# Kernel tuning notes

Hardware: AMD Instinct MI355X
Metric: run time of the kernel (lower is better)

## Reference

```python
import jax, jax.numpy as jnp
import numpy as np

B, NB, BIN = 8, 512, 10           # batch, num_bins, bin_size
D, H, L, F, E, K = 1024, 8, 4, 1024, 30, 4  # emb, heads, layers, ffn, experts, top_k
S = NB + 1                        # seq len with CLS token
DH = D // H
CAP = 1152


def _pos_encoding(seq, d):
    pos = np.arange(seq)[:, None].astype(np.float32)
    div = np.exp(np.arange(0, d, 2).astype(np.float32) * (-np.log(10000.0) / d))
    pe = np.zeros((seq, d), dtype=np.float32)
    pe[:, 0::2] = np.sin(pos * div)
    pe[:, 1::2] = np.cos(pos * div)
    return jnp.asarray(pe)

PE = _pos_encoding(S, D)


def _ln(h, g, b):
    m = h.mean(-1, keepdims=True)
    v = ((h - m) ** 2).mean(-1, keepdims=True)
    return (h - m) * jax.lax.rsqrt(v + 1e-5) * g + b


def _conv(h, w, dil):
    # torch Conv1d(k=3, padding=dil, dilation=dil, bias=False) -> same length
    return jax.lax.conv_general_dilated(h, w, (1,), [(dil, dil)], rhs_dilation=(dil,),
                                        dimension_numbers=('NCH', 'OIH', 'NCH'))


def _moe(m, Wg, Bg, W1, B1, W2, B2):
    # top-k routed expert FFN with capacity-based dispatch (no dense all-expert compute)
    T = B * S
    xt = m.reshape(T, D)
    probs = jax.nn.softmax(xt @ Wg + Bg, axis=-1)           # [T, E]
    gate, idx = jax.lax.top_k(probs, K)                     # [T, K]
    gate = gate / gate.sum(-1, keepdims=True)
    e = idx.reshape(-1)                                     # [T*K]
    g = gate.reshape(-1)
    oh = jax.nn.one_hot(e, E, dtype=jnp.int32)
    pos = (jnp.cumsum(oh, axis=0) * oh).sum(-1) - 1         # position within expert
    keep = pos < CAP
    pos_c = jnp.where(keep, pos, CAP)                       # overflow -> dummy slot CAP
    xt_rep = xt[jnp.repeat(jnp.arange(T), K)]               # [T*K, D]
    buf = jnp.zeros((E, CAP + 1, D), m.dtype).at[e, pos_c].add(xt_rep)
    hid = jax.nn.gelu(jnp.einsum('ecd,edf->ecf', buf, W1) + B1[:, None, :], approximate=False)
    out = jnp.einsum('ecf,efd->ecd', hid, W2) + B2[:, None, :]
    y = out[e, pos_c] * (g * keep)[:, None]                 # dropped tokens masked to 0
    return y.reshape(T, K, D).sum(1).reshape(B, S, D)


def _layer(h, p):
    (l1g, l1b, l2g, l2b, Wq, Wk, Wv, Wo, Bq, Bk, Bv, Bo, Wg, Bg, We1, Be1, We2, Be2) = p
    a = _ln(h, l1g, l1b)
    q = (a @ Wq + Bq).reshape(B, S, H, DH)
    k = (a @ Wk + Bk).reshape(B, S, H, DH)
    v = (a @ Wv + Bv).reshape(B, S, H, DH)
    att = jax.nn.softmax(jnp.einsum('bqhd,bkhd->bhqk', q, k) / np.sqrt(DH), axis=-1)
    o = jnp.einsum('bhqk,bkhd->bqhd', att, v).reshape(B, S, D) @ Wo + Bo
    h = h + o
    m = _ln(h, l2g, l2b)
    h = h + _moe(m, Wg, Bg, We1, Be1, We2, Be2)
    return h, None


def _fwd(x, conv_w1, conv_w2, conv_w3, bn1_g, bn1_b, bn2_g, bn2_b, bn3_g, bn3_b,
         proj_w, proj_b, cls_token, mask_token, ln1_g, ln1_b, ln2_g, ln2_b,
         wq, wk, wv, wo, bq, bk, bv, bo, wg, bg, we1, be1, we2, be2):
    x3 = x.reshape(B, NB, BIN)
    h = x3.reshape(B * NB, 1, BIN)
    bn_scale = np.float32(1.0 / np.sqrt(1.0 + 1e-5))  # eval BN: running mean 0, var 1
    for w, gm, bt, dil in ((conv_w1, bn1_g, bn1_b, 1), (conv_w2, bn2_g, bn2_b, 2), (conv_w3, bn3_g, bn3_b, 4)):
        h = _conv(h, w, dil)
        h = h * (gm * bn_scale)[None, :, None] + bt[None, :, None]
        h = jax.nn.gelu(h, approximate=False)
    h = h.mean(-1)                                   # AdaptiveAvgPool1d(1)
    emb = (h @ proj_w + proj_b).reshape(B, NB, D)
    msk = jnp.all(x3 == -100.0, axis=-1)[..., None]
    emb = jnp.where(msk, mask_token, emb)
    emb = jnp.concatenate([jnp.broadcast_to(cls_token, (B, 1, D)), emb], axis=1)
    emb = emb + PE[None]
    h, _ = jax.lax.scan(_layer, emb, (ln1_g, ln1_b, ln2_g, ln2_b, wq, wk, wv, wo,
                                      bq, bk, bv, bo, wg, bg, we1, be1, we2, be2))
    return h[:, 0, :]


def setup_inputs() -> dict:
    key = jax.random.key(0)
    ks = iter(jax.random.split(key, 40))
    r = lambda shape, s=0.02: jax.random.normal(next(ks), shape, jnp.float32) * s
    return dict(
        x=jax.random.normal(next(ks), (B, NB * BIN), jnp.float32),
        conv_w1=r((16, 1, 3), 0.3), conv_w2=r((32, 16, 3), 0.15), conv_w3=r((64, 32, 3), 0.1),
        bn1_g=jnp.ones((16,)), bn1_b=jnp.zeros((16,)),
        bn2_g=jnp.ones((32,)), bn2_b=jnp.zeros((32,)),
        bn3_g=jnp.ones((64,)), bn3_b=jnp.zeros((64,)),
        proj_w=r((64, D), 0.05), proj_b=jnp.zeros((D,)),
        cls_token=r((1, 1, D)), mask_token=r((1, 1, D)),
        ln1_g=jnp.ones((L, D)), ln1_b=jnp.zeros((L, D)),
        ln2_g=jnp.ones((L, D)), ln2_b=jnp.zeros((L, D)),
        wq=r((L, D, D)), wk=r((L, D, D)), wv=r((L, D, D)), wo=r((L, D, D)),
        bq=jnp.zeros((L, D)), bk=jnp.zeros((L, D)), bv=jnp.zeros((L, D)), bo=jnp.zeros((L, D)),
        wg=r((L, D, E)), bg=jnp.zeros((L, E)),
        we1=r((L, E, D, F)), be1=jnp.zeros((L, E, F)),
        we2=r((L, E, F, D)), be2=jnp.zeros((L, E, D)),
    )


def reference(x, conv_w1, conv_w2, conv_w3, bn1_g, bn1_b, bn2_g, bn2_b, bn3_g, bn3_b,
              proj_w, proj_b, cls_token, mask_token, ln1_g, ln1_b, ln2_g, ln2_b,
              wq, wk, wv, wo, bq, bk, bv, bo, wg, bg, we1, be1, we2, be2):
    return _fwd(x, conv_w1, conv_w2, conv_w3, bn1_g, bn1_b, bn2_g, bn2_b, bn3_g, bn3_b,
                proj_w, proj_b, cls_token, mask_token, ln1_g, ln1_b, ln2_g, ln2_b,
                wq, wk, wv, wo, bq, bk, bv, bo, wg, bg, we1, be1, we2, be2)
```

## Files before the change

### kernel.cpp

```cpp
#include <hip/hip_runtime.h>
#include <hip/hip_bf16.h>
#include <math.h>

#define BATCH   8
#define NBINS   512
#define BINSZ   10
#define DMODEL  1024
#define NHEAD   8
#define DHEAD   128
#define NLAYER  4
#define NEXP    30
#define TOPK    4
#define SEQ     513
#define NTOK    (BATCH*SEQ)
#define NBINTOT (BATCH*NBINS)
#define CAPACITY 1152
#define TKF     (NTOK*TOPK)

typedef __attribute__((ext_vector_type(8))) __bf16 bf16x8;
typedef __attribute__((ext_vector_type(4))) float f32x4;

__device__ __forceinline__ float gelu_f(float x) {
  return 0.5f * x * (1.0f + erff(x * 0.7071067811865475f));
}

#define CSTEP(acc, T, DIL, hr, wA, wB, wC) { \
  float vv_ = (wB) * (hr)[T]; \
  if ((T) >= (DIL)) vv_ = fmaf((wA), (hr)[(T)-(DIL)], vv_); \
  if ((T) + (DIL) <= 9) vv_ = fmaf((wC), (hr)[(T)+(DIL)], vv_); \
  acc += vv_; }

#define CALL10(DIL, hr, wA, wB, wC) \
  CSTEP(t0,0,DIL,hr,wA,wB,wC); CSTEP(t1,1,DIL,hr,wA,wB,wC); \
  CSTEP(t2,2,DIL,hr,wA,wB,wC); CSTEP(t3,3,DIL,hr,wA,wB,wC); \
  CSTEP(t4,4,DIL,hr,wA,wB,wC); CSTEP(t5,5,DIL,hr,wA,wB,wC); \
  CSTEP(t6,6,DIL,hr,wA,wB,wC); CSTEP(t7,7,DIL,hr,wA,wB,wC); \
  CSTEP(t8,8,DIL,hr,wA,wB,wC); CSTEP(t9,9,DIL,hr,wA,wB,wC);

#define ZERO10 float t0=0.f,t1=0.f,t2=0.f,t3=0.f,t4=0.f,t5=0.f,t6=0.f,t7=0.f,t8=0.f,t9=0.f;

#define STORE10(dst, sc, sh) \
  (dst)[0]=gelu_f(t0*(sc)+(sh)); (dst)[1]=gelu_f(t1*(sc)+(sh)); \
  (dst)[2]=gelu_f(t2*(sc)+(sh)); (dst)[3]=gelu_f(t3*(sc)+(sh)); \
  (dst)[4]=gelu_f(t4*(sc)+(sh)); (dst)[5]=gelu_f(t5*(sc)+(sh)); \
  (dst)[6]=gelu_f(t6*(sc)+(sh)); (dst)[7]=gelu_f(t7*(sc)+(sh)); \
  (dst)[8]=gelu_f(t8*(sc)+(sh)); (dst)[9]=gelu_f(t9*(sc)+(sh));

__global__ __launch_bounds__(64) void conv_frontend(const float* __restrict__ x,
                              const float* __restrict__ w1, const float* __restrict__ w2,
                              const float* __restrict__ w3,
                              const float* __restrict__ g1, const float* __restrict__ b1,
                              const float* __restrict__ g2, const float* __restrict__ b2,
                              const float* __restrict__ g3, const float* __restrict__ b3,
                              float* __restrict__ feat, int* __restrict__ msk) {
  const float bnscale = 0.9999950000374997f;
  int bin = blockIdx.x;
  int c = threadIdx.x;
  __shared__ float xs[BINSZ];
  __shared__ float h1[16][BINSZ];
  __shared__ float h2[32][BINSZ];
  if (c < BINSZ) xs[c] = x[bin*BINSZ + c];
  if (c == 0) {
    int all = 1;
    for (int t = 0; t < BINSZ; t++) if (x[bin*BINSZ+t] != -100.0f) { all = 0; break; }
    msk[bin] = all;
  }
  __syncthreads();
  if (c < 16) {
    float sc = g1[c]*bnscale, sh = b1[c];
    float wA = w1[c*3], wB = w1[c*3+1], wC = w1[c*3+2];
    const float* hr = &xs[0];
    ZERO10;
    CALL10(1, hr, wA, wB, wC);
    STORE10(&h1[c][0], sc, sh);
  }
  __syncthreads();
  if (c < 32) {
    float sc = g2[c]*bnscale, sh = b2[c];
    ZERO10;
    for (int ci = 0; ci < 16; ci++) {
      const float* w = w2 + (c*16+ci)*3;
      float wA = w[0], wB = w[1], wC = w[2];
      const float* hr = &h1[ci][0];
      CALL10(2, hr, wA, wB, wC);
    }
    STORE10(&h2[c][0], sc, sh);
  }
  __syncthreads();
  {
    float sc = g3[c]*bnscale, sh = b3[c];
    ZERO10;
    for (int ci = 0; ci < 32; ci++) {
      const float* w = w3 + (c*32+ci)*3;
      float wA = w[0], wB = w[1], wC = w[2];
      const float* hr = &h2[ci][0];
      CALL10(4, hr, wA, wB, wC);
    }
    float mean = gelu_f(t0*sc+sh) + gelu_f(t1*sc+sh) + gelu_f(t2*sc+sh)
               + gelu_f(t3*sc+sh) + gelu_f(t4*sc+sh) + gelu_f(t5*sc+sh)
               + gelu_f(t6*sc+sh) + gelu_f(t7*sc+sh) + gelu_f(t8*sc+sh)
               + gelu_f(t9*sc+sh);
    feat[bin*64 + c] = mean * 0.1f;
  }
}

__global__ void embed_kernel(const float* __restrict__ feat, const int* __restrict__ msk,
                             const float* __restrict__ proj_w, const float* __restrict__ proj_b,
                             const float* __restrict__ cls_token, const float* __restrict__ mask_token,
                             float* __restrict__ h) {
  int s_ = blockIdx.x;
  int b  = blockIdx.y;
  int tid = threadIdx.x;
  __shared__ __align__(16) float fs[64];
  float out[4];
  if (s_ == 0) {
#pragma unroll
    for (int u = 0; u < 4; u++) out[u] = cls_token[tid*4+u];
  } else {
    int bin = b*NBINS + (s_-1);
    if (tid < 16) ((float4*)fs)[tid] = ((const float4*)(feat + (size_t)bin*64))[tid];
    __syncthreads();
    int m_ = msk[bin];
#pragma unroll
    for (int u = 0; u < 4; u++) {
      int d = tid*4+u;
      float acc = proj_b[d];
      for (int ci = 0; ci < 64; ci++) acc = fmaf(fs[ci], proj_w[ci*DMODEL + d], acc);
      out[u] = m_ ? mask_token[d] : acc;
    }
  }
  const float c0 = -0.008994473019507992f;
#pragma unroll
  for (int u = 0; u < 4; u++) {
    int d = tid*4+u;
    float div = expf(c0 * (float)(d & ~1));
    float ang = (float)s_ * div;
    float pe = (d & 1) ? cosf(ang) : sinf(ang);
    h[((size_t)(b*SEQ + s_))*DMODEL + d] = out[u] + pe;
  }
}

__global__ void ln_kernel(const float* __restrict__ x, float* __restrict__ out,
                          const float* __restrict__ g, const float* __restrict__ b) {
  int t = blockIdx.x, tid = threadIdx.x;
  float4 v = ((const float4*)(x + (size_t)t*DMODEL))[tid];
  float s  = v.x+v.y+v.z+v.w;
  float sq = v.x*v.x+v.y*v.y+v.z*v.z+v.w*v.w;
  for (int off = 32; off; off >>= 1) { s += __shfl_down(s, off); sq += __shfl_down(sq, off); }
  __shared__ float ss[4], ssq[4], mv[2];
  int w = tid >> 6, l = tid & 63;
  if (l == 0) { ss[w] = s; ssq[w] = sq; }
  __syncthreads();
  if (tid == 0) {
    float a = 0, c = 0;
    for (int i = 0; i < 4; i++) { a += ss[i]; c += ssq[i]; }
    float mean = a * (1.f/DMODEL);
    float var  = c * (1.f/DMODEL) - mean*mean;
    mv[0] = mean; mv[1] = rsqrtf(var + 1e-5f);
  }
  __syncthreads();
  float mean = mv[0], inv = mv[1];
  float4 gg = ((const float4*)g)[tid];
  float4 bb = ((const float4*)b)[tid];
  float4 o;
  o.x = (v.x-mean)*inv*gg.x + bb.x;
  o.y = (v.y-mean)*inv*gg.y + bb.y;
  o.z = (v.z-mean)*inv*gg.z + bb.z;
  o.w = (v.w-mean)*inv*gg.w + bb.w;
  ((float4*)(out + (size_t)t*DMODEL))[tid] = o;
}

template<int MODE>
__global__ __launch_bounds__(512) void gemm_bf16(
    const float* __restrict__ A, const float* __restrict__ W,
    const float* __restrict__ bias, float* __restrict__ C, int M,
    const int* __restrict__ rowmap, const int* __restrict__ cnt,
    const float* __restrict__ gate) {
  int tid = threadIdx.x;
  int rowbase, validrows, e = 0;
  const float* Wb = W;
  if (MODE <= 1) {
    rowbase = blockIdx.x * 128;
    validrows = M - rowbase; if (validrows > 128) validrows = 128;
  } else {
    e = blockIdx.x / 9;
    int p0 = (blockIdx.x % 9) * 128;
    int ce = cnt[e];
    if (p0 >= ce) return;
    rowbase = p0;
    validrows = ce - p0; if (validrows > 128) validrows = 128;
    Wb = W + (size_t)e * 1024 * 1024;
  }
  int colbase = blockIdx.y * 128;

  __shared__ __align__(16) __bf16 As[4][128][8];
  __shared__ __align__(16) __bf16 Bs[4][128][8];
  __shared__ int srcrow[128];
  __shared__ int frow[128];

  if (tid < 128) {
    if (MODE <= 1) { srcrow[tid] = rowbase + tid; frow[tid] = rowbase + tid; }
    else if (tid < validrows) {
      int f = rowmap[e*CAPACITY + rowbase + tid];
      frow[tid] = f;
      srcrow[tid] = (MODE == 2) ? (f >> 2) : f;
    } else { frow[tid] = 0; srcrow[tid] = 0; }
  }
  __syncthreads();

  int arow = tid >> 2, ag = tid & 3;
  int wcol = tid & 127, wgp = tid >> 7;
  bool aval = (arow < validrows);
  const float* Ap = A + (size_t)srcrow[arow] * 1024 + ag * 8;
  const float* Wp = Wb + (size_t)(wgp * 8) * 1024 + colbase + wcol;

  int w  = tid >> 6;
  int wr = w & 3, wc = w >> 2;
  int l  = tid & 63;
  int lr = l & 15, lg = l >> 4;

  f32x4 acc[2][4] = {};

  float4 a_lo = {}, a_hi = {};
  float wreg[8];
  if (aval) { a_lo = *(const float4*)(Ap); a_hi = *(const float4*)(Ap + 4); }
#pragma unroll
  for (int j = 0; j < 8; j++) wreg[j] = Wp[(size_t)j * 1024];

  for (int kt = 0; kt < 1024; kt += 32) {
    __syncthreads();
    bf16x8 av;
    av[0] = (__bf16)a_lo.x; av[1] = (__bf16)a_lo.y; av[2] = (__bf16)a_lo.z; av[3] = (__bf16)a_lo.w;
    av[4] = (__bf16)a_hi.x; av[5] = (__bf16)a_hi.y; av[6] = (__bf16)a_hi.z; av[7] = (__bf16)a_hi.w;
    *(bf16x8*)&As[ag][arow][0] = av;
    bf16x8 bv;
#pragma unroll
    for (int j = 0; j < 8; j++) bv[j] = (__bf16)wreg[j];
    *(bf16x8*)&Bs[wgp][wcol][0] = bv;
    __syncthreads();

    if (kt + 32 < 1024) {
      if (aval) {
        a_lo = *(const float4*)(Ap + kt + 32);
        a_hi = *(const float4*)(Ap + kt + 36);
      }
#pragma unroll
      for (int j = 0; j < 8; j++) wreg[j] = Wp[(size_t)(kt + 32 + j) * 1024];
    }

    bf16x8 af[2], bf[4];
    af[0] = *(const bf16x8*)&As[lg][wr*32 + lr][0];
    af[1] = *(const bf16x8*)&As[lg][wr*32 + 16 + lr][0];
#pragma unroll
    for (int fj = 0; fj < 4; fj++) bf[fj] = *(const bf16x8*)&Bs[lg][wc*64 + fj*16 + lr][0];
#pragma unroll
    for (int fi = 0; fi < 2; fi++)
#pragma unroll
      for (int fj = 0; fj < 4; fj++)
        acc[fi][fj] = __builtin_amdgcn_mfma_f32_16x16x32_bf16(af[fi], bf[fj], acc[fi][fj], 0, 0, 0);
  }

  const float* bptr = (MODE >= 2) ? (bias + (size_t)e * 1024) : bias;
#pragma unroll
  for (int fj = 0; fj < 4; fj++) {
    int col = wc*64 + fj*16 + lr;
    float bvv = bptr[colbase + col];
#pragma unroll
    for (int fi = 0; fi < 2; fi++) {
#pragma unroll
      for (int i = 0; i < 4; i++) {
        int r = wr*32 + fi*16 + lg*4 + i;
        if (r >= validrows) continue;
        float val = acc[fi][fj][i] + bvv;
        if (MODE == 0) {
          C[(size_t)(rowbase + r)*1024 + colbase + col] = val;
        } else if (MODE == 1) {
          float* p = C + (size_t)(rowbase + r)*1024 + colbase + col;
          *p = *p + val;
        } else if (MODE == 2) {
          C[(size_t)frow[r]*1024 + colbase + col] = gelu_f(val);
        } else {
          C[(size_t)frow[r]*1024 + colbase + col] = gate[frow[r]] * val;
        }
      }
    }
  }
}

__global__ __launch_bounds__(256) void attn_mfma(const float* __restrict__ q,
                                                 const float* __restrict__ k,
                                                 const float* __restrict__ v,
                                                 float* __restrict__ o) {
  int qt = blockIdx.x;
  int bh = blockIdx.y;
  int b = bh >> 3, hh = bh & 7;
  int tid = threadIdx.x;
  int wid = tid >> 6, l = tid & 63;
  int lr = l & 15, lg = l >> 4;

  __shared__ __align__(16) __bf16 Ks[64*128];
  __shared__ __align__(16) __bf16 Vt[128*64];

  const float scale = 0.08838834764831845f;

  int qtok = qt*64 + wid*16 + lr;
  int qtokc = qtok < SEQ ? qtok : SEQ-1;
  const float* qrow = q + ((size_t)(b*SEQ + qtokc))*DMODEL + hh*DHEAD;
  bf16x8 qf[4];
#pragma unroll
  for (int c = 0; c < 4; c++) {
    float4 x0 = *(const float4*)(qrow + c*32 + lg*8);
    float4 x1 = *(const float4*)(qrow + c*32 + lg*8 + 4);
    bf16x8 t;
    t[0]=(__bf16)x0.x; t[1]=(__bf16)x0.y; t[2]=(__bf16)x0.z; t[3]=(__bf16)x0.w;
    t[4]=(__bf16)x1.x; t[5]=(__bf16)x1.y; t[6]=(__bf16)x1.z; t[7]=(__bf16)x1.w;
    qf[c] = t;
  }

  float mreg = -1e30f, lsum = 0.f;
  f32x4 Oacc[8] = {};

  int krow = tid & 63, kdc = tid >> 6;
  int vd = tid & 127, vkg0 = tid >> 7;

  for (int kt = 0; kt < 9; kt++) {
    int kt0 = kt*64;
    __syncthreads();
    {
      int tok = kt0 + krow; if (tok >= SEQ) tok = SEQ-1;
      const float* kr = k + ((size_t)(b*SEQ + tok))*DMODEL + hh*DHEAD + kdc*32;
#pragma unroll
      for (int s2 = 0; s2 < 4; s2++) {
        float4 a0 = *(const float4*)(kr + s2*8);
        float4 a1 = *(const float4*)(kr + s2*8 + 4);
        bf16x8 t;
        t[0]=(__bf16)a0.x; t[1]=(__bf16)a0.y; t[2]=(__bf16)a0.z; t[3]=(__bf16)a0.w;
        t[4]=(__bf16)a1.x; t[5]=(__bf16)a1.y; t[6]=(__bf16)a1.z; t[7]=(__bf16)a1.w;
        int byte = (krow*256 + (kdc*32 + s2*8)*2) ^ ((krow & 7) << 4);
        *(bf16x8*)((char*)Ks + byte) = t;
      }
    }
    {
#pragma unroll
      for (int it = 0; it < 4; it++) {
        int kkg = vkg0 + it*2;
        bf16x8 t;
#pragma unroll
        for (int j = 0; j < 8; j++) {
          int tok = kt0 + kkg*8 + j; if (tok >= SEQ) tok = SEQ-1;
          t[j] = (__bf16)v[((size_t)(b*SEQ + tok))*DMODEL + hh*DHEAD + vd];
        }
        int byte = (vd*128 + kkg*16) ^ ((vd & 7) << 4);
        *(bf16x8*)((char*)Vt + byte) = t;
      }
    }
    __syncthreads();

    f32x4 sacc[4] = {};
#pragma unroll
    for (int c = 0; c < 4; c++) {
#pragma unroll
      for (int jb = 0; jb < 4; jb++) {
        int row = jb*16 + lr;
        int byte = (row*256 + (c*32 + lg*8)*2) ^ ((lr & 7) << 4);
        bf16x8 af = *(const bf16x8*)((const char*)Ks + byte);
        sacc[jb] = __builtin_amdgcn_mfma_f32_16x16x32_bf16(af, qf[c], sacc[jb], 0, 0, 0);
      }
    }

    float sv[4][4];
    float mt = -1e30f;
#pragma unroll
    for (int jb = 0; jb < 4; jb++)
#pragma unroll
      for (int i = 0; i < 4; i++) {
        int kkI = kt0 + jb*16 + lg*4 + i;
        float s = sacc[jb][i] * scale;
        if (kkI >= SEQ) s = -1e30f;
        sv[jb][i] = s;
        mt = fmaxf(mt, s);
      }
    mt = fmaxf(mt, __shfl_xor(mt, 16));
    mt = fmaxf(mt, __shfl_xor(mt, 32));
    float mnew = fmaxf(mreg, mt);
    float alpha = expf(mreg - mnew);
    float rs = 0.f;
#pragma unroll
    for (int jb = 0; jb < 4; jb++)
#pragma unroll
      for (int i = 0; i < 4; i++) {
        float p = expf(sv[jb][i] - mnew);
        sv[jb][i] = p; rs += p;
      }
    rs += __shfl_xor(rs, 16);
    rs += __shfl_xor(rs, 32);
    lsum = lsum * alpha + rs;
    mreg = mnew;

    unsigned pk[4][2];
#pragma unroll
    for (int jb = 0; jb < 4; jb++) {
      unsigned short c0 = __builtin_bit_cast(unsigned short, (__bf16)sv[jb][0]);
      unsigned short c1 = __builtin_bit_cast(unsigned short, (__bf16)sv[jb][1]);
      unsigned short c2 = __builtin_bit_cast(unsigned short, (__bf16)sv[jb][2]);
      unsigned short c3 = __builtin_bit_cast(unsigned short, (__bf16)sv[jb][3]);
      pk[jb][0] = ((unsigned)c1 << 16) | c0;
      pk[jb][1] = ((unsigned)c3 << 16) | c2;
    }

    float al0 = __shfl(alpha, lg*4 + 0);
    float al1 = __shfl(alpha, lg*4 + 1);
    float al2 = __shfl(alpha, lg*4 + 2);
    float al3 = __shfl(alpha, lg*4 + 3);
#pragma unroll
    for (int db = 0; db < 8; db++) {
      Oacc[db][0] *= al0; Oacc[db][1] *= al1; Oacc[db][2] *= al2; Oacc[db][3] *= al3;
    }

    int srcA = lr + ((lg & 1) << 5);
    int srcB = srcA + 16;
    bool hiSel = (lg >> 1) != 0;
#pragma unroll
    for (int c = 0; c < 2; c++) {
      int a00 = __shfl((int)pk[2*c][0], srcA);
      int a01 = __shfl((int)pk[2*c][1], srcA);
      int a10 = __shfl((int)pk[2*c+1][0], srcA);
      int a11 = __shfl((int)pk[2*c+1][1], srcA);
      int b00 = __shfl((int)pk[2*c][0], srcB);
      int b01 = __shfl((int)pk[2*c][1], srcB);
      int b10 = __shfl((int)pk[2*c+1][0], srcB);
      int b11 = __shfl((int)pk[2*c+1][1], srcB);
      int4 pa;
      pa.x = hiSel ? a10 : a00;
      pa.y = hiSel ? a11 : a01;
      pa.z = hiSel ? b10 : b00;
      pa.w = hiSel ? b11 : b01;
      bf16x8 paf = __builtin_bit_cast(bf16x8, pa);
#pragma unroll
      for (int db = 0; db < 8; db++) {
        int d = db*16 + lr;
        int byte = (d*128 + (c*32 + lg*8)*2) ^ ((lr & 7) << 4);
        bf16x8 bfv = *(const bf16x8*)((const char*)Vt + byte);
        Oacc[db] = __builtin_amdgcn_mfma_f32_16x16x32_bf16(paf, bfv, Oacc[db], 0, 0, 0);
      }
    }
  }

  float l0 = __shfl(lsum, lg*4 + 0);
  float l1 = __shfl(lsum, lg*4 + 1);
  float l2 = __shfl(lsum, lg*4 + 2);
  float l3 = __shfl(lsum, lg*4 + 3);
  float inv[4] = {1.f/l0, 1.f/l1, 1.f/l2, 1.f/l3};
#pragma unroll
  for (int i = 0; i < 4; i++) {
    int tok = qt*64 + wid*16 + lg*4 + i;
    if (tok < SEQ) {
      float* dst = o + ((size_t)(b*SEQ + tok))*DMODEL + hh*DHEAD + lr;
#pragma unroll
      for (int db = 0; db < 8; db++) dst[db*16] = Oacc[db][i] * inv[i];
    }
  }
}

__global__ void moe_gate(const float* __restrict__ m, const float* __restrict__ wg,
                         const float* __restrict__ bg, int* __restrict__ idx,
                         float* __restrict__ gate) {
  int t = blockIdx.x, tid = threadIdx.x;
  __shared__ __align__(16) float xs[DMODEL];
  __shared__ float probs[32];
  ((float4*)xs)[tid] = ((const float4*)(m + (size_t)t*DMODEL))[tid];
  __syncthreads();
  int e = tid >> 3, sub = tid & 7;
  if (e < NEXP) {
    float p = 0.f;
    for (int d = sub; d < DMODEL; d += 8) p = fmaf(xs[d], wg[d*NEXP + e], p);
    p += __shfl_down(p, 4, 8);
    p += __shfl_down(p, 2, 8);
    p += __shfl_down(p, 1, 8);
    if (sub == 0) probs[e] = p + bg[e];
  }
  __syncthreads();
  if (tid == 0) {
    float mx = probs[0];
    for (int i = 1; i < NEXP; i++) mx = fmaxf(mx, probs[i]);
    float ssum = 0.f;
    for (int i = 0; i < NEXP; i++) { probs[i] = expf(probs[i]-mx); ssum += probs[i]; }
    float invs = 1.f / ssum;
    float gv[TOPK]; int gi[TOPK]; float gsum = 0.f;
    for (int kk = 0; kk < TOPK; kk++) {
      float best = -1.f; int bi = 0;
      for (int i = 0; i < NEXP; i++) if (probs[i] > best) { best = probs[i]; bi = i; }
      gv[kk] = best * invs; gi[kk] = bi; probs[bi] = -1.f; gsum += gv[kk];
    }
    float ginv = 1.f / gsum;
    for (int kk = 0; kk < TOPK; kk++) { idx[t*TOPK+kk] = gi[kk]; gate[t*TOPK+kk] = gv[kk]*ginv; }
  }
}

__global__ void moe_dispatch(const int* __restrict__ idx, int* __restrict__ slot,
                             int* __restrict__ rowmap, int* __restrict__ cnt) {
  int e = blockIdx.x, tid = threadIdx.x;
  int lane = tid & 63, wid = tid >> 6;
  __shared__ int wsum[4];
  int base = 0;
  for (int c0 = 0; c0 < TKF; c0 += 256) {
    int f = c0 + tid;
    int match = (f < TKF && idx[f] == e) ? 1 : 0;
    unsigned long long bal = __ballot(match);
    if (lane == 0) wsum[wid] = __popcll(bal);
    __syncthreads();
    int prefix = 0;
#pragma unroll
    for (int w2 = 0; w2 < 4; w2++) if (w2 < wid) prefix += wsum[w2];
    int total = wsum[0] + wsum[1] + wsum[2] + wsum[3];
    if (match) {
      int pos = base + prefix + __popcll(bal & ((1ull << lane) - 1ull));
      if (pos < CAPACITY) { slot[f] = pos; rowmap[e*CAPACITY + pos] = f; }
      else slot[f] = -1;
    }
    base += total;
    __syncthreads();
  }
  if (tid == 0) cnt[e] = (base < CAPACITY) ? base : CAPACITY;
}

__global__ void moe_sum(const float* __restrict__ y, const int* __restrict__ slot,
                        float* __restrict__ h) {
  int t = blockIdx.x, d4 = threadIdx.x;
  float4 acc = ((float4*)(h + (size_t)t*DMODEL))[d4];
#pragma unroll
  for (int kk = 0; kk < TOPK; kk++) {
    int f = t*TOPK + kk;
    if (slot[f] >= 0) {
      float4 yv = ((const float4*)(y + (size_t)f*DMODEL))[d4];
      acc.x += yv.x; acc.y += yv.y; acc.z += yv.z; acc.w += yv.w;
    }
  }
  ((float4*)(h + (size_t)t*DMODEL))[d4] = acc;
}

__global__ void final_copy(const float* __restrict__ h, float* __restrict__ out) {
  int b = blockIdx.x, tid = threadIdx.x;
  float4 v = ((const float4*)(h + (size_t)b*SEQ*DMODEL))[tid];
  ((float4*)(out + (size_t)b*DMODEL))[tid] = v;
}

extern "C" void kernel_launch(void* const* d_in, const int* in_sizes, int n_in,
                              void* d_out, int out_size, void* d_ws, size_t ws_size,
                              hipStream_t stream) {
  (void)in_sizes; (void)n_in; (void)out_size; (void)ws_size;
  const float* x         = (const float*)d_in[0];
  const float* conv_w1   = (const float*)d_in[1];
  const float* conv_w2   = (const float*)d_in[2];
  const float* conv_w3   = (const float*)d_in[3];
  const float* bn1_g     = (const float*)d_in[4];
  const float* bn1_b     = (const float*)d_in[5];
  const float* bn2_g     = (const float*)d_in[6];
  const float* bn2_b     = (const float*)d_in[7];
  const float* bn3_g     = (const float*)d_in[8];
  const float* bn3_b     = (const float*)d_in[9];
  const float* proj_w    = (const float*)d_in[10];
  const float* proj_b    = (const float*)d_in[11];
  const float* cls_token = (const float*)d_in[12];
  const float* mask_tok  = (const float*)d_in[13];
  const float* ln1_g     = (const float*)d_in[14];
  const float* ln1_b     = (const float*)d_in[15];
  const float* ln2_g     = (const float*)d_in[16];
  const float* ln2_b     = (const float*)d_in[17];
  const float* wq        = (const float*)d_in[18];
  const float* wk        = (const float*)d_in[19];
  const float* wv        = (const float*)d_in[20];
  const float* wo        = (const float*)d_in[21];
  const float* bq        = (const float*)d_in[22];
  const float* bk        = (const float*)d_in[23];
  const float* bv        = (const float*)d_in[24];
  const float* bo        = (const float*)d_in[25];
  const float* wg        = (const float*)d_in[26];
  const float* bg        = (const float*)d_in[27];
  const float* we1       = (const float*)d_in[28];
  const float* be1       = (const float*)d_in[29];
  const float* we2       = (const float*)d_in[30];
  const float* be2       = (const float*)d_in[31];
  float* out = (float*)d_out;

  float* ws = (float*)d_ws;
  const size_t TD = (size_t)NTOK * DMODEL;
  float* h    = ws;
  float* xbuf = ws + TD;
  float* qb   = ws + 2*TD;
  float* kb   = ws + 3*TD;
  float* vb   = ws + 4*TD;
  float* ao   = ws + 5*TD;
  float* hid  = ws + 2*TD;
  float* yb   = ws + 6*TD;
  float* feat = ws + 10*TD;
  float* gate = feat + (size_t)NBINTOT*64;
  int* idx    = (int*)(gate + TKF);
  int* slot   = idx + TKF;
  int* rowmap = slot + TKF;
  int* cnt    = rowmap + NEXP*CAPACITY;
  int* msk    = cnt + 32;

  conv_frontend<<<NBINTOT, 64, 0, stream>>>(x, conv_w1, conv_w2, conv_w3,
      bn1_g, bn1_b, bn2_g, bn2_b, bn3_g, bn3_b, feat, msk);
  embed_kernel<<<dim3(SEQ, BATCH), 256, 0, stream>>>(feat, msk, proj_w, proj_b,
      cls_token, mask_tok, h);

  dim3 gdense((NTOK + 127)/128, 8);
  dim3 gmoe(NEXP*9, 8);

  for (int l = 0; l < NLAYER; l++) {
    const float* wq_l = wq + (size_t)l*DMODEL*DMODEL;
    const float* wk_l = wk + (size_t)l*DMODEL*DMODEL;
    const float* wv_l = wv + (size_t)l*DMODEL*DMODEL;
    const float* wo_l = wo + (size_t)l*DMODEL*DMODEL;
    const float* we1_l = we1 + (size_t)l*NEXP*DMODEL*1024;
    const float* we2_l = we2 + (size_t)l*NEXP*1024*DMODEL;

    ln_kernel<<<NTOK, 256, 0, stream>>>(h, xbuf, ln1_g + (size_t)l*DMODEL, ln1_b + (size_t)l*DMODEL);
    gemm_bf16<0><<<gdense, 512, 0, stream>>>(xbuf, wq_l, bq + (size_t)l*DMODEL, qb, NTOK, nullptr, nullptr, nullptr);
    gemm_bf16<0><<<gdense, 512, 0, stream>>>(xbuf, wk_l, bk + (size_t)l*DMODEL, kb, NTOK, nullptr, nullptr, nullptr);
    gemm_bf16<0><<<gdense, 512, 0, stream>>>(xbuf, wv_l, bv + (size_t)l*DMODEL, vb, NTOK, nullptr, nullptr, nullptr);
    attn_mfma<<<dim3(9, BATCH*NHEAD), 256, 0, stream>>>(qb, kb, vb, ao);
    gemm_bf16<1><<<gdense, 512, 0, stream>>>(ao, wo_l, bo + (size_t)l*DMODEL, h, NTOK, nullptr, nullptr, nullptr);
    ln_kernel<<<NTOK, 256, 0, stream>>>(h, xbuf, ln2_g + (size_t)l*DMODEL, ln2_b + (size_t)l*DMODEL);
    moe_gate<<<NTOK, 256, 0, stream>>>(xbuf, wg + (size_t)l*DMODEL*NEXP, bg + (size_t)l*NEXP, idx, gate);
    moe_dispatch<<<NEXP, 256, 0, stream>>>(idx, slot, rowmap, cnt);
    gemm_bf16<2><<<gmoe, 512, 0, stream>>>(xbuf, we1_l, be1 + (size_t)l*NEXP*1024, hid, 0, rowmap, cnt, nullptr);
    gemm_bf16<3><<<gmoe, 512, 0, stream>>>(hid, we2_l, be2 + (size_t)l*NEXP*1024, yb, 0, rowmap, cnt, gate);
    moe_sum<<<NTOK, 256, 0, stream>>>(yb, slot, h);
  }
  final_copy<<<BATCH, 256, 0, stream>>>(h, out);
}
```

Baseline: 3.000 ms.

## Store activations and transposed weights in bf16 to halve GEMM and attention traffic

Adds a per-call kernel that transposes every weight matrix to K-contiguous bf16 layout. The layernorm also writes a bf16 copy of its output. GEMMs, attention and the MoE hidden buffer now read and write bf16 intermediates, so the per-tile float-to-bf16 conversions disappear and strided weight loads become vector loads. The cost is a transpose pass over all weights on every call (about 1 GB of fp32 read), extra workspace, and bf16 rounding of q/k/v and hidden activations.

```diff
diff --git a/kernel.cpp b/kernel.cpp
--- a/kernel.cpp
+++ b/kernel.cpp
@@ -18,10 +18,42 @@
 #define TKF     (NTOK*TOPK)
 
 typedef __attribute__((ext_vector_type(8))) __bf16 bf16x8;
+typedef __attribute__((ext_vector_type(4))) __bf16 bf16x4;
 typedef __attribute__((ext_vector_type(4))) float f32x4;
 
 __device__ __forceinline__ float gelu_f(float x) {
   return 0.5f * x * (1.0f + erff(x * 0.7071067811865475f));
+}
+
+__device__ __forceinline__ bf16x8 bf8_zero() {
+  int4 z = make_int4(0, 0, 0, 0);
+  return __builtin_bit_cast(bf16x8, z);
+}
+
+__global__ __launch_bounds__(256) void transpose_w(const float* __restrict__ src,
+                                                   __bf16* __restrict__ dst) {
+  int mat = blockIdx.y;
+  int tile = blockIdx.x;
+  int kt = (tile >> 4) * 64;
+  int nt = (tile & 15) * 64;
+  const float* s = src + (size_t)mat * 1024 * 1024;
+  __bf16* d = dst + (size_t)mat * 1024 * 1024;
+  __shared__ float t[64][65];
+  int tid = threadIdx.x;
+  int r = tid >> 4, c4 = (tid & 15) * 4;
+#pragma unroll
+  for (int i = 0; i < 4; i++) {
+    float4 v = *(const float4*)(s + (size_t)(kt + r + i*16) * 1024 + nt + c4);
+    t[r + i*16][c4+0] = v.x; t[r + i*16][c4+1] = v.y;
+    t[r + i*16][c4+2] = v.z; t[r + i*16][c4+3] = v.w;
+  }
+  __syncthreads();
+  int r2 = tid >> 2, c2 = (tid & 3) * 16;
+  bf16x8 o0, o1;
+#pragma unroll
+  for (int j = 0; j < 8; j++) { o0[j] = (__bf16)t[c2+j][r2]; o1[j] = (__bf16)t[c2+8+j][r2]; }
+  *(bf16x8*)(d + (size_t)(nt + r2) * 1024 + kt + c2)     = o0;
+  *(bf16x8*)(d + (size_t)(nt + r2) * 1024 + kt + c2 + 8) = o1;
 }
 
 #define CSTEP(acc, T, DIL, hr, wA, wB, wC) { \
@@ -141,6 +173,7 @@
 }
 
 __global__ void ln_kernel(const float* __restrict__ x, float* __restrict__ out,
+                          __bf16* __restrict__ outb,
                           const float* __restrict__ g, const float* __restrict__ b) {
   int t = blockIdx.x, tid = threadIdx.x;
   float4 v = ((const float4*)(x + (size_t)t*DMODEL))[tid];
@@ -168,17 +201,20 @@
   o.z = (v.z-mean)*inv*gg.z + bb.z;
   o.w = (v.w-mean)*inv*gg.w + bb.w;
   ((float4*)(out + (size_t)t*DMODEL))[tid] = o;
+  bf16x4 ob;
+  ob[0] = (__bf16)o.x; ob[1] = (__bf16)o.y; ob[2] = (__bf16)o.z; ob[3] = (__bf16)o.w;
+  *(bf16x4*)(outb + (size_t)t*DMODEL + tid*4) = ob;
 }
 
 template<int MODE>
 __global__ __launch_bounds__(512) void gemm_bf16(
-    const float* __restrict__ A, const float* __restrict__ W,
-    const float* __restrict__ bias, float* __restrict__ C, int M,
+    const __bf16* __restrict__ A, const __bf16* __restrict__ Wt,
+    const float* __restrict__ bias, void* __restrict__ C, int M,
     const int* __restrict__ rowmap, const int* __restrict__ cnt,
     const float* __restrict__ gate) {
   int tid = threadIdx.x;
   int rowbase, validrows, e = 0;
-  const float* Wb = W;
+  const __bf16* Wb = Wt;
   if (MODE <= 1) {
     rowbase = blockIdx.x * 128;
     validrows = M - rowbase; if (validrows > 128) validrows = 128;
@@ -189,7 +225,7 @@
     if (p0 >= ce) return;
     rowbase = p0;
     validrows = ce - p0; if (validrows > 128) validrows = 128;
-    Wb = W + (size_t)e * 1024 * 1024;
+    Wb = Wt + (size_t)e * 1024 * 1024;
   }
   int colbase = blockIdx.y * 128;
 
@@ -211,8 +247,8 @@
   int arow = tid >> 2, ag = tid & 3;
   int wcol = tid & 127, wgp = tid >> 7;
   bool aval = (arow < validrows);
-  const float* Ap = A + (size_t)srcrow[arow] * 1024 + ag * 8;
-  const float* Wp = Wb + (size_t)(wgp * 8) * 1024 + colbase + wcol;
+  const __bf16* Ap = A + (size_t)srcrow[arow] * 1024 + ag * 8;
+  const __bf16* Wp = Wb + (size_t)(colbase + wcol) * 1024 + wgp * 8;
 
   int w  = tid >> 6;
   int wr = w & 3, wc = w >> 2;
@@ -221,31 +257,19 @@
 
   f32x4 acc[2][4] = {};
 
-  float4 a_lo = {}, a_hi = {};
-  float wreg[8];
-  if (aval) { a_lo = *(const float4*)(Ap); a_hi = *(const float4*)(Ap + 4); }
-#pragma unroll
-  for (int j = 0; j < 8; j++) wreg[j] = Wp[(size_t)j * 1024];
+  bf16x8 areg = bf8_zero(), breg;
+  if (aval) areg = *(const bf16x8*)(Ap);
+  breg = *(const bf16x8*)(Wp);
 
   for (int kt = 0; kt < 1024; kt += 32) {
     __syncthreads();
-    bf16x8 av;
-    av[0] = (__bf16)a_lo.x; av[1] = (__bf16)a_lo.y; av[2] = (__bf16)a_lo.z; av[3] = (__bf16)a_lo.w;
-    av[4] = (__bf16)a_hi.x; av[5] = (__bf16)a_hi.y; av[6] = (__bf16)a_hi.z; av[7] = (__bf16)a_hi.w;
-    *(bf16x8*)&As[ag][arow][0] = av;
-    bf16x8 bv;
-#pragma unroll
-    for (int j = 0; j < 8; j++) bv[j] = (__bf16)wreg[j];
-    *(bf16x8*)&Bs[wgp][wcol][0] = bv;
+    *(bf16x8*)&As[ag][arow][0] = areg;
+    *(bf16x8*)&Bs[wgp][wcol][0] = breg;
     __syncthreads();
 
     if (kt + 32 < 1024) {
-      if (aval) {
-        a_lo = *(const float4*)(Ap + kt + 32);
-        a_hi = *(const float4*)(Ap + kt + 36);
-      }
-#pragma unroll
-      for (int j = 0; j < 8; j++) wreg[j] = Wp[(size_t)(kt + 32 + j) * 1024];
+      if (aval) areg = *(const bf16x8*)(Ap + kt + 32);
+      breg = *(const bf16x8*)(Wp + kt + 32);
     }
 
     bf16x8 af[2], bf[4];
@@ -273,24 +297,24 @@
         if (r >= validrows) continue;
         float val = acc[fi][fj][i] + bvv;
         if (MODE == 0) {
-          C[(size_t)(rowbase + r)*1024 + colbase + col] = val;
+          ((__bf16*)C)[(size_t)(rowbase + r)*1024 + colbase + col] = (__bf16)val;
         } else if (MODE == 1) {
-          float* p = C + (size_t)(rowbase + r)*1024 + colbase + col;
+          float* p = (float*)C + (size_t)(rowbase + r)*1024 + colbase + col;
           *p = *p + val;
         } else if (MODE == 2) {
-          C[(size_t)frow[r]*1024 + colbase + col] = gelu_f(val);
+          ((__bf16*)C)[(size_t)frow[r]*1024 + colbase + col] = (__bf16)gelu_f(val);
         } else {
-          C[(size_t)frow[r]*1024 + colbase + col] = gate[frow[r]] * val;
+          ((float*)C)[(size_t)frow[r]*1024 + colbase + col] = gate[frow[r]] * val;
         }
       }
     }
   }
 }
 
-__global__ __launch_bounds__(256) void attn_mfma(const float* __restrict__ q,
-                                                 const float* __restrict__ k,
-                                                 const float* __restrict__ v,
-                                                 float* __restrict__ o) {
+__global__ __launch_bounds__(256) void attn_mfma(const __bf16* __restrict__ q,
+                                                 const __bf16* __restrict__ k,
+                                                 const __bf16* __restrict__ v,
+                                                 __bf16* __restrict__ o) {
   int qt = blockIdx.x;
   int bh = blockIdx.y;
   int b = bh >> 3, hh = bh & 7;
@@ -305,17 +329,10 @@
 
   int qtok = qt*64 + wid*16 + lr;
   int qtokc = qtok < SEQ ? qtok : SEQ-1;
-  const float* qrow = q + ((size_t)(b*SEQ + qtokc))*DMODEL + hh*DHEAD;
+  const __bf16* qrow = q + ((size_t)(b*SEQ + qtokc))*DMODEL + hh*DHEAD;
   bf16x8 qf[4];
 #pragma unroll
-  for (int c = 0; c < 4; c++) {
-    float4 x0 = *(const float4*)(qrow + c*32 + lg*8);
-    float4 x1 = *(const float4*)(qrow + c*32 + lg*8 + 4);
-    bf16x8 t;
-    t[0]=(__bf16)x0.x; t[1]=(__bf16)x0.y; t[2]=(__bf16)x0.z; t[3]=(__bf16)x0.w;
-    t[4]=(__bf16)x1.x; t[5]=(__bf16)x1.y; t[6]=(__bf16)x1.z; t[7]=(__bf16)x1.w;
-    qf[c] = t;
-  }
+  for (int c = 0; c < 4; c++) qf[c] = *(const bf16x8*)(qrow + c*32 + lg*8);
 
   float mreg = -1e30f, lsum = 0.f;
   f32x4 Oacc[8] = {};
@@ -328,14 +345,10 @@
     __syncthreads();
     {
       int tok = kt0 + krow; if (tok >= SEQ) tok = SEQ-1;
-      const float* kr = k + ((size_t)(b*SEQ + tok))*DMODEL + hh*DHEAD + kdc*32;
+      const __bf16* kr = k + ((size_t)(b*SEQ + tok))*DMODEL + hh*DHEAD + kdc*32;
 #pragma unroll
       for (int s2 = 0; s2 < 4; s2++) {
-        float4 a0 = *(const float4*)(kr + s2*8);
-        float4 a1 = *(const float4*)(kr + s2*8 + 4);
-        bf16x8 t;
-        t[0]=(__bf16)a0.x; t[1]=(__bf16)a0.y; t[2]=(__bf16)a0.z; t[3]=(__bf16)a0.w;
-        t[4]=(__bf16)a1.x; t[5]=(__bf16)a1.y; t[6]=(__bf16)a1.z; t[7]=(__bf16)a1.w;
+        bf16x8 t = *(const bf16x8*)(kr + s2*8);
         int byte = (krow*256 + (kdc*32 + s2*8)*2) ^ ((krow & 7) << 4);
         *(bf16x8*)((char*)Ks + byte) = t;
       }
@@ -348,7 +361,7 @@
 #pragma unroll
         for (int j = 0; j < 8; j++) {
           int tok = kt0 + kkg*8 + j; if (tok >= SEQ) tok = SEQ-1;
-          t[j] = (__bf16)v[((size_t)(b*SEQ + tok))*DMODEL + hh*DHEAD + vd];
+          t[j] = v[((size_t)(b*SEQ + tok))*DMODEL + hh*DHEAD + vd];
         }
         int byte = (vd*128 + kkg*16) ^ ((vd & 7) << 4);
         *(bf16x8*)((char*)Vt + byte) = t;
@@ -455,9 +468,9 @@
   for (int i = 0; i < 4; i++) {
     int tok = qt*64 + wid*16 + lg*4 + i;
     if (tok < SEQ) {
-      float* dst = o + ((size_t)(b*SEQ + tok))*DMODEL + hh*DHEAD + lr;
-#pragma unroll
-      for (int db = 0; db < 8; db++) dst[db*16] = Oacc[db][i] * inv[i];
+      __bf16* dst = o + ((size_t)(b*SEQ + tok))*DMODEL + hh*DHEAD + lr;
+#pragma unroll
+      for (int db = 0; db < 8; db++) dst[db*16] = (__bf16)(Oacc[db][i] * inv[i]);
     }
   }
 }
@@ -583,23 +596,40 @@
   const float* be2       = (const float*)d_in[31];
   float* out = (float*)d_out;
 
-  float* ws = (float*)d_ws;
-  const size_t TD = (size_t)NTOK * DMODEL;
-  float* h    = ws;
-  float* xbuf = ws + TD;
-  float* qb   = ws + 2*TD;
-  float* kb   = ws + 3*TD;
-  float* vb   = ws + 4*TD;
-  float* ao   = ws + 5*TD;
-  float* hid  = ws + 2*TD;
-  float* yb   = ws + 6*TD;
-  float* feat = ws + 10*TD;
-  float* gate = feat + (size_t)NBINTOT*64;
-  int* idx    = (int*)(gate + TKF);
-  int* slot   = idx + TKF;
-  int* rowmap = slot + TKF;
-  int* cnt    = rowmap + NEXP*CAPACITY;
-  int* msk    = cnt + 32;
+  char* base = (char*)d_ws;
+  const size_t TDB = (size_t)NTOK * DMODEL * 4;
+  float*  h    = (float*)(base);
+  float*  xbuf = (float*)(base + TDB);
+  float*  yb   = (float*)(base + 2*TDB);
+  __bf16* xbf  = (__bf16*)(base + 6*TDB);
+  __bf16* qb   = (__bf16*)(base + 6*TDB + TDB/2);
+  __bf16* kb   = (__bf16*)(base + 7*TDB);
+  __bf16* vb   = (__bf16*)(base + 7*TDB + TDB/2);
+  __bf16* ao   = (__bf16*)(base + 8*TDB);
+  __bf16* hid  = (__bf16*)(base + 8*TDB + TDB/2);
+  char* misc   = base + 11*TDB;
+  float* feat  = (float*)misc;
+  float* gate  = feat + (size_t)NBINTOT*64;
+  int* idx     = (int*)(gate + TKF);
+  int* slot    = idx + TKF;
+  int* rowmap  = slot + TKF;
+  int* cnt     = rowmap + NEXP*CAPACITY;
+  int* msk     = cnt + 32;
+  char* wtb    = base + 12*TDB;
+  const size_t MB1 = (size_t)1024*1024;
+  __bf16* wtq  = (__bf16*)wtb;
+  __bf16* wtk  = wtq + 4*MB1;
+  __bf16* wtv  = wtk + 4*MB1;
+  __bf16* wto  = wtv + 4*MB1;
+  __bf16* wte1 = wto + 4*MB1;
+  __bf16* wte2 = wte1 + 120*MB1;
+
+  transpose_w<<<dim3(256, 4),   256, 0, stream>>>(wq,  wtq);
+  transpose_w<<<dim3(256, 4),   256, 0, stream>>>(wk,  wtk);
+  transpose_w<<<dim3(256, 4),   256, 0, stream>>>(wv,  wtv);
+  transpose_w<<<dim3(256, 4),   256, 0, stream>>>(wo,  wto);
+  transpose_w<<<dim3(256, 120), 256, 0, stream>>>(we1, wte1);
+  transpose_w<<<dim3(256, 120), 256, 0, stream>>>(we2, wte2);
 
   conv_frontend<<<NBINTOT, 64, 0, stream>>>(x, conv_w1, conv_w2, conv_w3,
       bn1_g, bn1_b, bn2_g, bn2_b, bn3_g, bn3_b, feat, msk);
@@ -610,24 +640,25 @@
   dim3 gmoe(NEXP*9, 8);
 
   for (int l = 0; l < NLAYER; l++) {
-    const float* wq_l = wq + (size_t)l*DMODEL*DMODEL;
-    const float* wk_l = wk + (size_t)l*DMODEL*DMODEL;
-    const float* wv_l = wv + (size_t)l*DMODEL*DMODEL;
-    const float* wo_l = wo + (size_t)l*DMODEL*DMODEL;
-    const float* we1_l = we1 + (size_t)l*NEXP*DMODEL*1024;
-    const float* we2_l = we2 + (size_t)l*NEXP*1024*DMODEL;
-
-    ln_kernel<<<NTOK, 256, 0, stream>>>(h, xbuf, ln1_g + (size_t)l*DMODEL, ln1_b + (size_t)l*DMODEL);
-    gemm_bf16<0><<<gdense, 512, 0, stream>>>(xbuf, wq_l, bq + (size_t)l*DMODEL, qb, NTOK, nullptr, nullptr, nullptr);
-    gemm_bf16<0><<<gdense, 512, 0, stream>>>(xbuf, wk_l, bk + (size_t)l*DMODEL, kb, NTOK, nullptr, nullptr, nullptr);
-    gemm_bf16<0><<<gdense, 512, 0, stream>>>(xbuf, wv_l, bv + (size_t)l*DMODEL, vb, NTOK, nullptr, nullptr, nullptr);
+    for (int z = 0; z < 1; z++) {}
+    __bf16* wtq_l = wtq + (size_t)l*MB1;
+    __bf16* wtk_l = wtk + (size_t)l*MB1;
+    __bf16* wtv_l = wtv + (size_t)l*MB1;
+    __bf16* wto_l = wto + (size_t)l*MB1;
+    __bf16* wte1_l = wte1 + (size_t)l*NEXP*MB1;
+    __bf16* wte2_l = wte2 + (size_t)l*NEXP*MB1;
+
+    ln_kernel<<<NTOK, 256, 0, stream>>>(h, xbuf, xbf, ln1_g + (size_t)l*DMODEL, ln1_b + (size_t)l*DMODEL);
+    gemm_bf16<0><<<gdense, 512, 0, stream>>>(xbf, wtq_l, bq + (size_t)l*DMODEL, qb, NTOK, nullptr, nullptr, nullptr);
+    gemm_bf16<0><<<gdense, 512, 0, stream>>>(xbf, wtk_l, bk + (size_t)l*DMODEL, kb, NTOK, nullptr, nullptr, nullptr);
+    gemm_bf16<0><<<gdense, 512, 0, stream>>>(xbf, wtv_l, bv + (size_t)l*DMODEL, vb, NTOK, nullptr, nullptr, nullptr);
     attn_mfma<<<dim3(9, BATCH*NHEAD), 256, 0, stream>>>(qb, kb, vb, ao);
-    gemm_bf16<1><<<gdense, 512, 0, stream>>>(ao, wo_l, bo + (size_t)l*DMODEL, h, NTOK, nullptr, nullptr, nullptr);
-    ln_kernel<<<NTOK, 256, 0, stream>>>(h, xbuf, ln2_g + (size_t)l*DMODEL, ln2_b + (size_t)l*DMODEL);
+    gemm_bf16<1><<<gdense, 512, 0, stream>>>(ao, wto_l, bo + (size_t)l*DMODEL, h, NTOK, nullptr, nullptr, nullptr);
+    ln_kernel<<<NTOK, 256, 0, stream>>>(h, xbuf, xbf, ln2_g + (size_t)l*DMODEL, ln2_b + (size_t)l*DMODEL);
     moe_gate<<<NTOK, 256, 0, stream>>>(xbuf, wg + (size_t)l*DMODEL*NEXP, bg + (size_t)l*NEXP, idx, gate);
     moe_dispatch<<<NEXP, 256, 0, stream>>>(idx, slot, rowmap, cnt);
-    gemm_bf16<2><<<gmoe, 512, 0, stream>>>(xbuf, we1_l, be1 + (size_t)l*NEXP*1024, hid, 0, rowmap, cnt, nullptr);
-    gemm_bf16<3><<<gmoe, 512, 0, stream>>>(hid, we2_l, be2 + (size_t)l*NEXP*1024, yb, 0, rowmap, cnt, gate);
+    gemm_bf16<2><<<gmoe, 512, 0, stream>>>(xbf, wte1_l, be1 + (size_t)l*NEXP*1024, hid, 0, rowmap, cnt, nullptr);
+    gemm_bf16<3><<<gmoe, 512, 0, stream>>>(hid, wte2_l, be2 + (size_t)l*NEXP*1024, yb, 0, rowmap, cnt, gate);
     moe_sum<<<NTOK, 256, 0, stream>>>(yb, slot, h);
   }
   final_copy<<<BATCH, 256, 0, stream>>>(h, out);
```

Result: faster. 2.778 ms (-7.4%).
